# Performance work log

Hardware: AMD Instinct MI355X
Metric: run time of the kernel (lower is better)

Reference implementation:

```python
import jax, jax.numpy as jnp
import numpy as np

H = 16        # num query heads
HKV = 4       # num kv heads
D = 128       # head_dim
HID = 2048    # hidden_size
G = H // HKV  # heads per kv group


def setup_inputs() -> dict:
    key = jax.random.key(0)
    ks = jax.random.split(key, 9)
    s = 0.02
    x = jax.random.normal(ks[0], (2, 2048, HID), dtype=jnp.float32)
    wq = jax.random.normal(ks[1], (HID, H * D), dtype=jnp.float32) * s
    bq = jnp.zeros((H * D,), jnp.float32)
    wk = jax.random.normal(ks[2], (HID, HKV * D), dtype=jnp.float32) * s
    bk = jnp.zeros((HKV * D,), jnp.float32)
    wv = jax.random.normal(ks[3], (HID, HKV * D), dtype=jnp.float32) * s
    bv = jnp.zeros((HKV * D,), jnp.float32)
    wo = jax.random.normal(ks[4], (HID, HID), dtype=jnp.float32) * s
    bo = jnp.zeros((HID,), jnp.float32)
    return dict(x=x, wq=wq, bq=bq, wk=wk, bk=bk, wv=wv, bv=bv, wo=wo, bo=bo)


def reference(x, wq, bq, wk, bk, wv, bv, wo, bo):
    B, S, _ = x.shape
    scale = jnp.float32(1.0 / np.sqrt(D))
    # projections (torch Linear with weight stored as [in, out] here)
    q = (x @ wq + bq).reshape(B, S, H, D)          # [B,S,H,D]
    k = (x @ wk + bk).reshape(B, S, HKV, D)        # [B,S,Hkv,D]
    v = (x @ wv + bv).reshape(B, S, HKV, D)
    # group query heads by kv head instead of expanding KV
    q = q.reshape(B, S, HKV, G, D)
    scores = jnp.einsum('bqhgd,bkhd->bhgqk', q, k) * scale  # [B,Hkv,G,S,S]
    causal = jnp.triu(jnp.ones((S, S), dtype=bool), k=1)
    scores = jnp.where(causal, jnp.float32(-1e9), scores)
    weights = jax.nn.softmax(scores, axis=-1)
    out = jnp.einsum('bhgqk,bkhd->bqhgd', weights, v)        # [B,S,Hkv,G,D]
    out = out.reshape(B, S, H * D)
    return out @ wo + bo
```

## Files before the change

kernel.cpp:

```cpp
#include <hip/hip_runtime.h>
#include <hip/hip_bf16.h>
#include <math.h>

#define HID 2048
#define NH 16
#define NKV 4
#define HD 128
#define GQ 4
#define BATCH 2

typedef short short8v __attribute__((ext_vector_type(8)));
typedef float f32x4 __attribute__((ext_vector_type(4)));

__device__ __forceinline__ ushort f2bf(float f) {
  uint u = __float_as_uint(f);
  uint r = (u + 0x7fffu + ((u >> 16) & 1u)) >> 16;
  return (ushort)r;
}

__device__ __forceinline__ uint cvt_pk_bf16(float lo, float hi) {
  uint r;
  asm("v_cvt_pk_bf16_f32 %0, %1, %2" : "=v"(r) : "v"(lo), "v"(hi));
  return r;
}

__device__ __forceinline__ void gld_lds16(const void* g, void* lds) {
  __builtin_amdgcn_global_load_lds(
      (const __attribute__((address_space(1))) unsigned int*)g,
      (__attribute__((address_space(3))) unsigned int*)lds, 16, 0, 0);
}

#define WAVE_LDS_FENCE()                                \
  do {                                                  \
    asm volatile("s_waitcnt lgkmcnt(0)" ::: "memory");  \
    __builtin_amdgcn_sched_barrier(0);                  \
  } while (0)

__device__ const int QT_TAB[24] = {7, 8, 9, 10, 11, 12, 13, 14, 15, 15, 6, 14,
                                   5, 13, 4, 12, 3, 11, 2, 10, 1, 9, 0, 8};
__device__ const int LO_TAB[24] = {0, 0, 0, 0, 0, 0, 0, 0, 0, 16, 0, 16,
                                   0, 16, 0, 16, 0, 16, 0, 16, 0, 16, 0, 16};

__global__ __launch_bounds__(256) void castx_kernel(
    const float* __restrict__ x, ushort* __restrict__ xb) {
  const int i = ((int)blockIdx.x * 256 + (int)threadIdx.x) * 8;
  float4 f0 = *reinterpret_cast<const float4*>(x + i);
  float4 f1 = *reinterpret_cast<const float4*>(x + i + 4);
  uint4 o;
  o.x = (uint)f2bf(f0.x) | ((uint)f2bf(f0.y) << 16);
  o.y = (uint)f2bf(f0.z) | ((uint)f2bf(f0.w) << 16);
  o.z = (uint)f2bf(f1.x) | ((uint)f2bf(f1.y) << 16);
  o.w = (uint)f2bf(f1.z) | ((uint)f2bf(f1.w) << 16);
  *reinterpret_cast<uint4*>(xb + i) = o;
}

__global__ __launch_bounds__(256) void tcast_kernel(
    const float* __restrict__ W, ushort* __restrict__ Wt, int K, int N) {
  __shared__ float T[32][33];
  const int k0 = blockIdx.x * 32;
  const int n0 = blockIdx.y * 32;
  const int t = threadIdx.x;
  const int r = t >> 3;
  const int c4 = (t & 7) * 4;
  float4 vin = *reinterpret_cast<const float4*>(
      &W[(size_t)(k0 + r) * N + n0 + c4]);
  T[c4 + 0][r] = vin.x;
  T[c4 + 1][r] = vin.y;
  T[c4 + 2][r] = vin.z;
  T[c4 + 3][r] = vin.w;
  __syncthreads();
  ushort4 o;
  o.x = f2bf(T[r][c4 + 0]);
  o.y = f2bf(T[r][c4 + 1]);
  o.z = f2bf(T[r][c4 + 2]);
  o.w = f2bf(T[r][c4 + 3]);
  *reinterpret_cast<ushort4*>(&Wt[(size_t)(n0 + r) * K + k0 + c4]) = o;
}

__global__ __launch_bounds__(256) void merge_kernel(
    const float* __restrict__ OaccA, const float* __restrict__ OaccB,
    const float* __restrict__ LaccA, const float* __restrict__ LaccB,
    ushort* __restrict__ attnb) {
  const int i = (int)blockIdx.x * 256 + (int)threadIdx.x;
  const int d8 = i & 15;
  const int h = (i >> 4) & 15;
  const int r = i >> 8;
  const float invl = 1.0f / (LaccA[r * NH + h] + LaccB[r * NH + h]);
  const size_t off = ((size_t)r * (NH * HD)) + h * HD + d8 * 8;
  float4 a0 = *reinterpret_cast<const float4*>(OaccA + off);
  float4 a1 = *reinterpret_cast<const float4*>(OaccA + off + 4);
  float4 b0 = *reinterpret_cast<const float4*>(OaccB + off);
  float4 b1 = *reinterpret_cast<const float4*>(OaccB + off + 4);
  uint4 o;
  o.x = cvt_pk_bf16((a0.x + b0.x) * invl, (a0.y + b0.y) * invl);
  o.y = cvt_pk_bf16((a0.z + b0.z) * invl, (a0.w + b0.w) * invl);
  o.z = cvt_pk_bf16((a1.x + b1.x) * invl, (a1.y + b1.y) * invl);
  o.w = cvt_pk_bf16((a1.z + b1.z) * invl, (a1.w + b1.w) * invl);
  const int b = r >> 10;
  const int s = 1024 + (r & 1023);
  *reinterpret_cast<uint4*>(
      &attnb[((size_t)(b * 2048 + s)) * (NH * HD) + h * HD + d8 * 8]) = o;
}

template <int MODE>
__global__ __launch_bounds__(256) void gemm_big(
    const ushort* __restrict__ A,
    const ushort* __restrict__ W0, const ushort* __restrict__ W1,
    const ushort* __restrict__ W2,
    const float* __restrict__ b0, const float* __restrict__ b1,
    const float* __restrict__ b2,
    void* __restrict__ C0, void* __restrict__ C1, void* __restrict__ C2,
    int M, int K, int S) {
  __shared__ ushort As[3][128 * 32];
  __shared__ ushort Bs[3][128 * 32];
  const int tid = threadIdx.x;

  const int nbx = (int)gridDim.x;
  int bid = (int)blockIdx.y * nbx + (int)blockIdx.x;
  const int cpx = (nbx * (int)gridDim.y) >> 3;
  bid = (bid & 7) * cpx + (bid >> 3);
  const int m0 = (bid / nbx) * 128;
  const int n0 = (bid % nbx) * 128;

  const int wave = tid >> 6;
  const int lane = tid & 63;
  const int quad = lane >> 4;
  const int lr = lane & 15;
  const int l4 = lane >> 2;
  const int lc = (lane & 3) * 8;
  const int wm = (wave >> 1) * 64;
  const int wn = (wave & 1) * 64;

  const ushort* Wt;
  const float* bias;
  int nloc, Nout, om;
  void* Cout;
  if (MODE == 0) {
    Wt = W0; bias = b0; nloc = n0; Nout = 2048; om = 0; Cout = C0;
  } else {
    if (n0 < 2048)      { Wt = W0; bias = b0; nloc = n0;        Nout = 2048; om = 1; Cout = C0; }
    else if (n0 < 2560) { Wt = W1; bias = b1; nloc = n0 - 2048; Nout = 512;  om = 1; Cout = C1; }
    else                { Wt = W2; bias = b2; nloc = n0 - 2560; Nout = 512;  om = 2; Cout = C2; }
  }

  f32x4 acc[4][4];
#pragma unroll
  for (int i = 0; i < 4; ++i)
#pragma unroll
    for (int j = 0; j < 4; ++j) acc[i][j] = (f32x4){0.f, 0.f, 0.f, 0.f};

  const size_t rowA = (size_t)(m0 + wave * 32 + l4) * K + lc;
  const size_t rowB = (size_t)(nloc + wave * 32 + l4) * K + lc;

#define STAGE_GEMM(t, bi)                                                  \
  do {                                                                     \
    const int kof = (t) * 32;                                              \
    gld_lds16(&A[rowA + kof], &As[bi][(wave * 32) * 32]);                  \
    gld_lds16(&A[rowA + 16 * K + kof], &As[bi][(wave * 32 + 16) * 32]);    \
    gld_lds16(&Wt[rowB + kof], &Bs[bi][(wave * 32) * 32]);                 \
    gld_lds16(&Wt[rowB + 16 * K + kof], &Bs[bi][(wave * 32 + 16) * 32]);   \
  } while (0)

  const int nt = K / 32;
  STAGE_GEMM(0, 0);
  STAGE_GEMM(1, 1);

  for (int t = 0; t < nt; ++t) {
    const int cur = t % 3;
    __builtin_amdgcn_s_barrier();
    if (t + 2 < nt) {
      STAGE_GEMM(t + 2, (t + 2) % 3);
      asm volatile("s_waitcnt vmcnt(8)" ::: "memory");
    } else if (t + 1 < nt) {
      asm volatile("s_waitcnt vmcnt(4)" ::: "memory");
    } else {
      asm volatile("s_waitcnt vmcnt(0)" ::: "memory");
    }
    __builtin_amdgcn_s_barrier();
    __builtin_amdgcn_sched_barrier(0);

    short8v af[4], bf[4];
#pragma unroll
    for (int x = 0; x < 4; ++x) {
      const int ra = wm + x * 16 + lr;
      af[x] = *reinterpret_cast<const short8v*>(&As[cur][ra * 32 + quad * 8]);
      const int rb = wn + x * 16 + lr;
      bf[x] = *reinterpret_cast<const short8v*>(&Bs[cur][rb * 32 + quad * 8]);
    }
#pragma unroll
    for (int i = 0; i < 4; ++i)
#pragma unroll
      for (int j = 0; j < 4; ++j)
        acc[i][j] = __builtin_amdgcn_mfma_f32_16x16x32_bf16(
            af[i], bf[j], acc[i][j], 0, 0, 0);
  }
#undef STAGE_GEMM

#pragma unroll
  for (int i = 0; i < 4; ++i) {
    const int row_base = m0 + wm + i * 16 + quad * 4;
#pragma unroll
    for (int j = 0; j < 4; ++j) {
      const int col = nloc + wn + j * 16 + lr;
      const float b = bias[col];
      if (om == 0) {
        float* C = (float*)Cout;
#pragma unroll
        for (int rg = 0; rg < 4; ++rg)
          C[(size_t)(row_base + rg) * Nout + col] = acc[i][j][rg] + b;
      } else if (om == 1) {
        ushort* C = (ushort*)Cout;
#pragma unroll
        for (int rg = 0; rg < 4; ++rg)
          C[(size_t)(row_base + rg) * Nout + col] = f2bf(acc[i][j][rg] + b);
      } else {
        ushort* C = (ushort*)Cout;
        const int bb = (row_base >= S) ? 1 : 0;
        const int s = row_base - bb * S;
        const int kvh = col >> 7;
        const int d = col & 127;
        ushort4 o;
        o.x = f2bf(acc[i][j][0] + b);
        o.y = f2bf(acc[i][j][1] + b);
        o.z = f2bf(acc[i][j][2] + b);
        o.w = f2bf(acc[i][j][3] + b);
        *reinterpret_cast<ushort4*>(
            &C[((size_t)(bb * NKV + kvh) * HD + d) * S + s]) = o;
      }
    }
  }
}

__device__ __forceinline__ void stage_k8(const ushort* __restrict__ Kb,
                                         ushort* Kdst, int k0, int wave,
                                         int lane) {
  const int rK = lane >> 4, cK = lane & 15;
#pragma unroll
  for (int c = 0; c < 2; ++c) {
    const int g = wave * 2 + c;
    const int row = g * 4 + rK;
    const int jk = cK ^ (row & 15);
    gld_lds16(&Kb[(size_t)(k0 + row) * (NKV * HD) + jk * 8], &Kdst[g * 512]);
  }
}
__device__ __forceinline__ void stage_v8(const ushort* __restrict__ Vb,
                                         ushort* Vdst, int k0, int S, int wave,
                                         int lane) {
  const int rV = lane >> 3, cV = lane & 7;
#pragma unroll
  for (int c = 0; c < 2; ++c) {
    const int g = wave * 2 + c;
    const int d = g * 8 + rV;
    const int jv = cV ^ (d & 7);
    gld_lds16(&Vb[(size_t)d * S + k0 + jv * 8], &Vdst[g * 512]);
  }
}

__global__ __launch_bounds__(512, 4) void gqa_attn_mfma(
    const ushort* __restrict__ Qg, const ushort* __restrict__ Kgl,
    const ushort* __restrict__ Vt_g, ushort* __restrict__ O,
    float* __restrict__ OaccA, float* __restrict__ OaccB,
    float* __restrict__ LaccA, float* __restrict__ LaccB, int S) {
  __shared__ __align__(16) ushort L[24576];
  ushort* K0 = L;
  ushort* K1 = L + 8192;
  ushort* Vs = L + 16384;

  const int tid = threadIdx.x;
  const int wave = tid >> 6;
  const int lane = tid & 63;
  const int quad = lane >> 4;
  const int lr = lane & 15;
  const int item = blockIdx.z;
  const int qt = QT_TAB[item];
  const int lo = LO_TAB[item];
  const int ntf = 2 * qt + 2;
  const int hi = lo ? ntf : (ntf < 16 ? ntf : 16);
  const bool part = (qt >= 8);
  const int q0 = qt * 128;
  const int hq = blockIdx.x;
  const int b = blockIdx.y;
  const int kvh = hq >> 2;
  const float C = 0.12751745f;

  const ushort* Qb = Qg + ((size_t)b * S) * (NH * HD) + (size_t)hq * HD;
  const ushort* Kb = Kgl + ((size_t)b * S) * (NKV * HD) + (size_t)kvh * HD;
  const ushort* Vb = Vt_g + ((size_t)(b * NKV + kvh) * HD) * S;

#pragma unroll
  for (int i = 0; i < 4; ++i) {
    const int id = tid + i * 512;
    const int r = id >> 4, c = id & 15;
    const int p = c ^ (r & 15);
    *reinterpret_cast<uint4*>(&L[r * 128 + p * 8]) =
        *reinterpret_cast<const uint4*>(
            &Qb[(size_t)(q0 + r) * (NH * HD) + c * 8]);
  }
  __syncthreads();
  short8v aq[4];
  {
    const int ra = wave * 16 + lr;
#pragma unroll
    for (int ks = 0; ks < 4; ++ks)
      aq[ks] = *reinterpret_cast<const short8v*>(
          &L[ra * 128 + (((ks * 4 + quad) ^ lr) & 15) * 8]);
  }
  __syncthreads();

  f32x4 oacc[8];
#pragma unroll
  for (int nb = 0; nb < 8; ++nb) oacc[nb] = (f32x4){0.f, 0.f, 0.f, 0.f};
  float l_r = 0.f;

  const int laneA = ((quad * 2) & 3) * 16 + lr;
  const int laneB = ((quad * 2 + 1) & 3) * 16 + lr;
  const bool hihalf = (quad >= 2);

  stage_k8(Kb, (lo & 1) ? K1 : K0, lo * 64, wave, lane);

  for (int kt = lo; kt < hi; ++kt) {
    const int k0v = kt * 64;
    const ushort* Kc = (kt & 1) ? K1 : K0;

    __builtin_amdgcn_s_barrier();
    stage_v8(Vb, Vs, k0v, S, wave, lane);
    if (kt + 1 < hi) {
      stage_k8(Kb, (kt & 1) ? K0 : K1, k0v + 64, wave, lane);
      asm volatile("s_waitcnt vmcnt(4)" ::: "memory");
    } else {
      asm volatile("s_waitcnt vmcnt(2)" ::: "memory");
    }
    __builtin_amdgcn_s_barrier();
    __builtin_amdgcn_sched_barrier(0);

    f32x4 sacc[4];
    __builtin_amdgcn_s_setprio(1);
#pragma unroll
    for (int nb = 0; nb < 4; ++nb) {
      sacc[nb] = (f32x4){0.f, 0.f, 0.f, 0.f};
      const int rb = nb * 16 + lr;
#pragma unroll
      for (int ks = 0; ks < 4; ++ks) {
        short8v bk = *reinterpret_cast<const short8v*>(
            &Kc[rb * 128 + (((ks * 4 + quad) ^ lr) & 15) * 8]);
        sacc[nb] = __builtin_amdgcn_mfma_f32_16x16x32_bf16(
            bk, aq[ks], sacc[nb], 0, 0, 0);
      }
    }
    __builtin_amdgcn_s_setprio(0);

    const bool needmask = (kt >= 2 * qt);
    const int qi = q0 + wave * 16 + lr;
    uint u[4][2];
    float rs = 0.f;
#pragma unroll
    for (int nb = 0; nb < 4; ++nb) {
      float p[4];
#pragma unroll
      for (int rg = 0; rg < 4; ++rg) {
        float sv = sacc[nb][rg] * C;
        if (needmask) {
          const int kj = k0v + nb * 16 + quad * 4 + rg;
          if (kj > qi) sv = -1e30f;
        }
        p[rg] = __builtin_amdgcn_exp2f(sv);
        rs += p[rg];
      }
      u[nb][0] = cvt_pk_bf16(p[0], p[1]);
      u[nb][1] = cvt_pk_bf16(p[2], p[3]);
    }
    rs += __shfl_xor(rs, 16);
    rs += __shfl_xor(rs, 32);
    l_r += rs;

    short8v ap[2];
#pragma unroll
    for (int ks = 0; ks < 2; ++ks) {
      const uint w0a = __shfl(u[2 * ks + 0][0], laneA);
      const uint w0b = __shfl(u[2 * ks + 1][0], laneA);
      const uint w1a = __shfl(u[2 * ks + 0][1], laneA);
      const uint w1b = __shfl(u[2 * ks + 1][1], laneA);
      const uint w2a = __shfl(u[2 * ks + 0][0], laneB);
      const uint w2b = __shfl(u[2 * ks + 1][0], laneB);
      const uint w3a = __shfl(u[2 * ks + 0][1], laneB);
      const uint w3b = __shfl(u[2 * ks + 1][1], laneB);
      uint4 q4;
      q4.x = hihalf ? w0b : w0a;
      q4.y = hihalf ? w1b : w1a;
      q4.z = hihalf ? w2b : w2a;
      q4.w = hihalf ? w3b : w3a;
      ap[ks] = *reinterpret_cast<short8v*>(&q4);
    }

    if (kt + 1 < hi) {
      asm volatile("s_waitcnt vmcnt(2)" ::: "memory");
    } else {
      asm volatile("s_waitcnt vmcnt(0)" ::: "memory");
    }
    __builtin_amdgcn_s_barrier();
    __builtin_amdgcn_sched_barrier(0);

    __builtin_amdgcn_s_setprio(1);
#pragma unroll
    for (int nb = 0; nb < 8; ++nb) {
      const int rv = nb * 16 + lr;
#pragma unroll
      for (int ks = 0; ks < 2; ++ks) {
        short8v bv = *reinterpret_cast<const short8v*>(
            &Vs[rv * 64 + (((ks * 4 + quad) ^ lr) & 7) * 8]);
        oacc[nb] = __builtin_amdgcn_mfma_f32_16x16x32_bf16(
            ap[ks], bv, oacc[nb], 0, 0, 0);
      }
    }
    __builtin_amdgcn_s_setprio(0);
  }

  if (part) {
    float* Oacc = lo ? OaccB : OaccA;
    float* Lacc = lo ? LaccB : LaccA;
    float* Oa = Oacc +
                ((size_t)(b * 1024 + (q0 - 1024) + wave * 16 + quad * 4)) *
                    (NH * HD) +
                hq * HD;
#pragma unroll
    for (int nb = 0; nb < 8; ++nb)
#pragma unroll
      for (int rg = 0; rg < 4; ++rg)
        Oa[(size_t)rg * (NH * HD) + nb * 16 + lr] = oacc[nb][rg];
    if (quad == 0)
      Lacc[(size_t)(b * 1024 + (q0 - 1024) + wave * 16 + lr) * NH + hq] = l_r;
  } else {
    const float invl = 1.0f / l_r;
    float inv[4];
#pragma unroll
    for (int rg = 0; rg < 4; ++rg)
      inv[rg] = __shfl(invl, (lane & 48) | (quad * 4 + rg));
    __syncthreads();
    ushort* ow = &L[wave * 16 * 128];
#pragma unroll
    for (int nb = 0; nb < 8; ++nb)
#pragma unroll
      for (int rg = 0; rg < 4; ++rg)
        ow[(quad * 4 + rg) * 128 + nb * 16 + lr] =
            f2bf(oacc[nb][rg] * inv[rg]);
    WAVE_LDS_FENCE();
    ushort* Ob = O + ((size_t)b * S) * (NH * HD) + (size_t)hq * HD;
#pragma unroll
    for (int ii = 0; ii < 4; ++ii) {
      const int id = lane + ii * 64;
      const int r16 = id >> 4, c = id & 15;
      uint4 val = *reinterpret_cast<const uint4*>(&ow[r16 * 128 + c * 8]);
      *reinterpret_cast<uint4*>(
          &Ob[(size_t)(q0 + wave * 16 + r16) * (NH * HD) + c * 8]) = val;
    }
  }
}

extern "C" void kernel_launch(void* const* d_in, const int* in_sizes, int n_in,
                              void* d_out, int out_size, void* d_ws,
                              size_t ws_size, hipStream_t stream) {
  const float* x = (const float*)d_in[0];
  const float* wq = (const float*)d_in[1];
  const float* bq = (const float*)d_in[2];
  const float* wk = (const float*)d_in[3];
  const float* bk = (const float*)d_in[4];
  const float* wv = (const float*)d_in[5];
  const float* bv = (const float*)d_in[6];
  const float* wo = (const float*)d_in[7];
  const float* bo = (const float*)d_in[8];
  float* out = (float*)d_out;

  const int M = in_sizes[0] / HID;
  const int S = M / BATCH;

  char* w = (char*)d_ws;
  ushort* xb    = (ushort*)(w + 0);
  ushort* qb    = (ushort*)(w + (16u << 20));
  ushort* kb    = (ushort*)(w + (32u << 20));
  ushort* vT    = (ushort*)(w + (36u << 20));
  ushort* attnb = (ushort*)(w + (40u << 20));
  ushort* wqT   = (ushort*)(w + (56u << 20));
  ushort* wkT   = (ushort*)(w + (64u << 20));
  ushort* wvT   = (ushort*)(w + (66u << 20));
  ushort* woT   = (ushort*)(w + (68u << 20));
  float* OaccA = (float*)(w + 0);
  float* OaccB = out;
  float* LaccA = (float*)(w + (64u << 20));
  float* LaccB = (float*)(w + (66u << 20));

  dim3 blk(256);
  castx_kernel<<<dim3((M * HID) / (8 * 256)), blk, 0, stream>>>(x, xb);
  tcast_kernel<<<dim3(HID / 32, (NH * HD) / 32), blk, 0, stream>>>(
      wq, wqT, HID, NH * HD);
  tcast_kernel<<<dim3(HID / 32, (NKV * HD) / 32), blk, 0, stream>>>(
      wk, wkT, HID, NKV * HD);
  tcast_kernel<<<dim3(HID / 32, (NKV * HD) / 32), blk, 0, stream>>>(
      wv, wvT, HID, NKV * HD);
  tcast_kernel<<<dim3(HID / 32, HID / 32), blk, 0, stream>>>(
      wo, woT, HID, HID);

  gemm_big<1><<<dim3(3072 / 128, M / 128), blk, 0, stream>>>(
      xb, wqT, wkT, wvT, bq, bk, bv, qb, kb, vT, M, HID, S);

  gqa_attn_mfma<<<dim3(NH, BATCH, 24), dim3(512), 0, stream>>>(
      qb, kb, vT, attnb, OaccA, OaccB, LaccA, LaccB, S);

  merge_kernel<<<dim3(2048), blk, 0, stream>>>(
      OaccA, OaccB, LaccA, LaccB, attnb);

  gemm_big<0><<<dim3(HID / 128, M / 128), blk, 0, stream>>>(
      attnb, woT, nullptr, nullptr, bo, nullptr, nullptr,
      out, nullptr, nullptr, M, HID, S);
}
```

Before: 308.1 us.

## Fuse prep casts into one launch and merge split-KV partials in-kernel via atomics

The x cast and the four weight transpose-casts move into a single prep kernel, which also zeroes an accumulation region inside the output buffer. The attention kernel's split partial results are now accumulated with float atomicAdd, and a per-tile arrival counter lets the last-finishing block normalise and write the bf16 output, so the separate merge kernel is gone. This cuts launch count and the merge pass, at the cost of atomic traffic, a zero-fill pass, and reliance on correct fencing between the two split blocks.

```diff
diff --git a/kernel.cpp b/kernel.cpp
--- a/kernel.cpp
+++ b/kernel.cpp
@@ -41,65 +41,56 @@
 __device__ const int LO_TAB[24] = {0, 0, 0, 0, 0, 0, 0, 0, 0, 16, 0, 16,
                                    0, 16, 0, 16, 0, 16, 0, 16, 0, 16, 0, 16};
 
-__global__ __launch_bounds__(256) void castx_kernel(
-    const float* __restrict__ x, ushort* __restrict__ xb) {
-  const int i = ((int)blockIdx.x * 256 + (int)threadIdx.x) * 8;
-  float4 f0 = *reinterpret_cast<const float4*>(x + i);
-  float4 f1 = *reinterpret_cast<const float4*>(x + i + 4);
-  uint4 o;
-  o.x = (uint)f2bf(f0.x) | ((uint)f2bf(f0.y) << 16);
-  o.y = (uint)f2bf(f0.z) | ((uint)f2bf(f0.w) << 16);
-  o.z = (uint)f2bf(f1.x) | ((uint)f2bf(f1.y) << 16);
-  o.w = (uint)f2bf(f1.z) | ((uint)f2bf(f1.w) << 16);
-  *reinterpret_cast<uint4*>(xb + i) = o;
-}
-
-__global__ __launch_bounds__(256) void tcast_kernel(
-    const float* __restrict__ W, ushort* __restrict__ Wt, int K, int N) {
-  __shared__ float T[32][33];
-  const int k0 = blockIdx.x * 32;
-  const int n0 = blockIdx.y * 32;
+__global__ __launch_bounds__(256) void prep_kernel(
+    const float* __restrict__ x, ushort* __restrict__ xb,
+    const float* __restrict__ wq, ushort* __restrict__ wqT,
+    const float* __restrict__ wk, ushort* __restrict__ wkT,
+    const float* __restrict__ wv, ushort* __restrict__ wvT,
+    const float* __restrict__ wo, ushort* __restrict__ woT,
+    float4* __restrict__ zreg) {
+  const int bid = blockIdx.x;
   const int t = threadIdx.x;
-  const int r = t >> 3;
-  const int c4 = (t & 7) * 4;
-  float4 vin = *reinterpret_cast<const float4*>(
-      &W[(size_t)(k0 + r) * N + n0 + c4]);
-  T[c4 + 0][r] = vin.x;
-  T[c4 + 1][r] = vin.y;
-  T[c4 + 2][r] = vin.z;
-  T[c4 + 3][r] = vin.w;
-  __syncthreads();
-  ushort4 o;
-  o.x = f2bf(T[r][c4 + 0]);
-  o.y = f2bf(T[r][c4 + 1]);
-  o.z = f2bf(T[r][c4 + 2]);
-  o.w = f2bf(T[r][c4 + 3]);
-  *reinterpret_cast<ushort4*>(&Wt[(size_t)(n0 + r) * K + k0 + c4]) = o;
-}
-
-__global__ __launch_bounds__(256) void merge_kernel(
-    const float* __restrict__ OaccA, const float* __restrict__ OaccB,
-    const float* __restrict__ LaccA, const float* __restrict__ LaccB,
-    ushort* __restrict__ attnb) {
-  const int i = (int)blockIdx.x * 256 + (int)threadIdx.x;
-  const int d8 = i & 15;
-  const int h = (i >> 4) & 15;
-  const int r = i >> 8;
-  const float invl = 1.0f / (LaccA[r * NH + h] + LaccB[r * NH + h]);
-  const size_t off = ((size_t)r * (NH * HD)) + h * HD + d8 * 8;
-  float4 a0 = *reinterpret_cast<const float4*>(OaccA + off);
-  float4 a1 = *reinterpret_cast<const float4*>(OaccA + off + 4);
-  float4 b0 = *reinterpret_cast<const float4*>(OaccB + off);
-  float4 b1 = *reinterpret_cast<const float4*>(OaccB + off + 4);
-  uint4 o;
-  o.x = cvt_pk_bf16((a0.x + b0.x) * invl, (a0.y + b0.y) * invl);
-  o.y = cvt_pk_bf16((a0.z + b0.z) * invl, (a0.w + b0.w) * invl);
-  o.z = cvt_pk_bf16((a1.x + b1.x) * invl, (a1.y + b1.y) * invl);
-  o.w = cvt_pk_bf16((a1.z + b1.z) * invl, (a1.w + b1.w) * invl);
-  const int b = r >> 10;
-  const int s = 1024 + (r & 1023);
-  *reinterpret_cast<uint4*>(
-      &attnb[((size_t)(b * 2048 + s)) * (NH * HD) + h * HD + d8 * 8]) = o;
+  if (bid < 4096) {
+    const int i = (bid * 256 + t) * 8;
+    float4 f0 = *reinterpret_cast<const float4*>(x + i);
+    float4 f1 = *reinterpret_cast<const float4*>(x + i + 4);
+    uint4 o;
+    o.x = (uint)f2bf(f0.x) | ((uint)f2bf(f0.y) << 16);
+    o.y = (uint)f2bf(f0.z) | ((uint)f2bf(f0.w) << 16);
+    o.z = (uint)f2bf(f1.x) | ((uint)f2bf(f1.y) << 16);
+    o.w = (uint)f2bf(f1.z) | ((uint)f2bf(f1.w) << 16);
+    *reinterpret_cast<uint4*>(xb + i) = o;
+  } else if (bid < 14336) {
+    const float* W;
+    ushort* Wt;
+    int N, idx;
+    if (bid < 8192)       { W = wq; Wt = wqT; N = 2048; idx = bid - 4096; }
+    else if (bid < 9216)  { W = wk; Wt = wkT; N = 512;  idx = bid - 8192; }
+    else if (bid < 10240) { W = wv; Wt = wvT; N = 512;  idx = bid - 9216; }
+    else                  { W = wo; Wt = woT; N = 2048; idx = bid - 10240; }
+    const int K = 2048;
+    const int k0 = (idx & 63) * 32;
+    const int n0 = (idx >> 6) * 32;
+    __shared__ float T[32][33];
+    const int r = t >> 3;
+    const int c4 = (t & 7) * 4;
+    float4 vin = *reinterpret_cast<const float4*>(
+        &W[(size_t)(k0 + r) * N + n0 + c4]);
+    T[c4 + 0][r] = vin.x;
+    T[c4 + 1][r] = vin.y;
+    T[c4 + 2][r] = vin.z;
+    T[c4 + 3][r] = vin.w;
+    __syncthreads();
+    ushort4 o;
+    o.x = f2bf(T[r][c4 + 0]);
+    o.y = f2bf(T[r][c4 + 1]);
+    o.z = f2bf(T[r][c4 + 2]);
+    o.w = f2bf(T[r][c4 + 3]);
+    *reinterpret_cast<ushort4*>(&Wt[(size_t)(n0 + r) * K + k0 + c4]) = o;
+  } else {
+    const int zi = bid - 14336;
+    zreg[(size_t)zi * 256 + t] = (float4){0.f, 0.f, 0.f, 0.f};
+  }
 }
 
 template <int MODE>
@@ -259,9 +250,10 @@
 __global__ __launch_bounds__(512, 4) void gqa_attn_mfma(
     const ushort* __restrict__ Qg, const ushort* __restrict__ Kgl,
     const ushort* __restrict__ Vt_g, ushort* __restrict__ O,
-    float* __restrict__ OaccA, float* __restrict__ OaccB,
-    float* __restrict__ LaccA, float* __restrict__ LaccB, int S) {
+    float* __restrict__ Oacc, float* __restrict__ Lacc,
+    int* __restrict__ Flags, int S) {
   __shared__ __align__(16) ushort L[24576];
+  __shared__ int flagres;
   ushort* K0 = L;
   ushort* K1 = L + 8192;
   ushort* Vs = L + 16384;
@@ -416,19 +408,43 @@
   }
 
   if (part) {
-    float* Oacc = lo ? OaccB : OaccA;
-    float* Lacc = lo ? LaccB : LaccA;
-    float* Oa = Oacc +
-                ((size_t)(b * 1024 + (q0 - 1024) + wave * 16 + quad * 4)) *
-                    (NH * HD) +
+    const int rbase = b * 1024 + (q0 - 1024);
+    float* Oa = Oacc + ((size_t)(rbase + wave * 16 + quad * 4)) * (NH * HD) +
                 hq * HD;
 #pragma unroll
     for (int nb = 0; nb < 8; ++nb)
 #pragma unroll
       for (int rg = 0; rg < 4; ++rg)
-        Oa[(size_t)rg * (NH * HD) + nb * 16 + lr] = oacc[nb][rg];
+        atomicAdd(&Oa[(size_t)rg * (NH * HD) + nb * 16 + lr], oacc[nb][rg]);
     if (quad == 0)
-      Lacc[(size_t)(b * 1024 + (q0 - 1024) + wave * 16 + lr) * NH + hq] = l_r;
+      atomicAdd(&Lacc[(size_t)(rbase + wave * 16 + lr) * NH + hq], l_r);
+
+    asm volatile("s_waitcnt vmcnt(0)" ::: "memory");
+    __syncthreads();
+    if (tid == 0)
+      flagres = atomicAdd(&Flags[(b * NH + hq) * 8 + (qt - 8)], 1);
+    __syncthreads();
+    if (flagres == 1) {
+      __threadfence();
+      const int rr = tid >> 2;
+      const int d0 = (tid & 3) * 32;
+      const int r = rbase + rr;
+      const float invl = 1.0f / Lacc[(size_t)r * NH + hq];
+      const float* src = Oacc + (size_t)r * (NH * HD) + hq * HD + d0;
+      ushort* dst =
+          O + ((size_t)(b * S + q0 + rr)) * (NH * HD) + hq * HD + d0;
+#pragma unroll
+      for (int c2 = 0; c2 < 4; ++c2) {
+        float4 a0 = *reinterpret_cast<const float4*>(src + c2 * 8);
+        float4 a1 = *reinterpret_cast<const float4*>(src + c2 * 8 + 4);
+        uint4 o;
+        o.x = cvt_pk_bf16(a0.x * invl, a0.y * invl);
+        o.y = cvt_pk_bf16(a0.z * invl, a0.w * invl);
+        o.z = cvt_pk_bf16(a1.x * invl, a1.y * invl);
+        o.w = cvt_pk_bf16(a1.z * invl, a1.w * invl);
+        *reinterpret_cast<uint4*>(dst + c2 * 8) = o;
+      }
+    }
   } else {
     const float invl = 1.0f / l_r;
     float inv[4];
@@ -483,32 +499,20 @@
   ushort* wkT   = (ushort*)(w + (64u << 20));
   ushort* wvT   = (ushort*)(w + (66u << 20));
   ushort* woT   = (ushort*)(w + (68u << 20));
-  float* OaccA = (float*)(w + 0);
-  float* OaccB = out;
-  float* LaccA = (float*)(w + (64u << 20));
-  float* LaccB = (float*)(w + (66u << 20));
-
-  dim3 blk(256);
-  castx_kernel<<<dim3((M * HID) / (8 * 256)), blk, 0, stream>>>(x, xb);
-  tcast_kernel<<<dim3(HID / 32, (NH * HD) / 32), blk, 0, stream>>>(
-      wq, wqT, HID, NH * HD);
-  tcast_kernel<<<dim3(HID / 32, (NKV * HD) / 32), blk, 0, stream>>>(
-      wk, wkT, HID, NKV * HD);
-  tcast_kernel<<<dim3(HID / 32, (NKV * HD) / 32), blk, 0, stream>>>(
-      wv, wvT, HID, NKV * HD);
-  tcast_kernel<<<dim3(HID / 32, HID / 32), blk, 0, stream>>>(
-      wo, woT, HID, HID);
-
-  gemm_big<1><<<dim3(3072 / 128, M / 128), blk, 0, stream>>>(
+  float* Oacc = out;
+  float* Lacc = (float*)((char*)out + (16u << 20));
+  int* Flags  = (int*)((char*)out + (16u << 20) + (128u << 10));
+
+  prep_kernel<<<dim3(18465), dim3(256), 0, stream>>>(
+      x, xb, wq, wqT, wk, wkT, wv, wvT, wo, woT, (float4*)out);
+
+  gemm_big<1><<<dim3(3072 / 128, M / 128), dim3(256), 0, stream>>>(
       xb, wqT, wkT, wvT, bq, bk, bv, qb, kb, vT, M, HID, S);
 
   gqa_attn_mfma<<<dim3(NH, BATCH, 24), dim3(512), 0, stream>>>(
-      qb, kb, vT, attnb, OaccA, OaccB, LaccA, LaccB, S);
-
-  merge_kernel<<<dim3(2048), blk, 0, stream>>>(
-      OaccA, OaccB, LaccA, LaccB, attnb);
-
-  gemm_big<0><<<dim3(HID / 128, M / 128), blk, 0, stream>>>(
+      qb, kb, vT, attnb, Oacc, Lacc, Flags, S);
+
+  gemm_big<0><<<dim3(HID / 128, M / 128), dim3(256), 0, stream>>>(
       attnb, woT, nullptr, nullptr, bo, nullptr, nullptr,
       out, nullptr, nullptr, M, HID, S);
 }
```

After: 388.4 us. 26.1% more time.
